# Optimization experiments

Hardware: AMD Instinct MI355X
Metric: run time of the kernel (lower is better)

Reference implementation:

```python
import jax, jax.numpy as jnp
import numpy as np

NUM_SRC1, NUM_DST1 = 2_000_000, 131_072
NUM_SRC2, NUM_DST2 = 131_072, 8_192
E1, E2 = NUM_DST1 * 15, NUM_DST2 * 15
F_IN, F_H = 128, 128


def setup_inputs() -> dict:
    key = jax.random.key(0)
    ks = jax.random.split(key, 10)
    return {
        "x": jax.random.normal(ks[0], (NUM_SRC1, F_IN), dtype=jnp.float32),
        "edge1_src": jax.random.randint(ks[1], (E1,), 0, NUM_SRC1, dtype=jnp.int32),
        "edge1_dst": jax.random.randint(ks[2], (E1,), 0, NUM_DST1, dtype=jnp.int32),
        "edge2_src": jax.random.randint(ks[3], (E2,), 0, NUM_SRC2, dtype=jnp.int32),
        "edge2_dst": jax.random.randint(ks[4], (E2,), 0, NUM_DST2, dtype=jnp.int32),
        "num_dst1": NUM_DST1,
        "num_dst2": NUM_DST2,
        "W_self1": jax.random.normal(ks[5], (F_IN, F_H), dtype=jnp.float32) * 0.05,
        "W_neigh1": jax.random.normal(ks[6], (F_IN, F_H), dtype=jnp.float32) * 0.05,
        "b1": jnp.zeros((F_H,), dtype=jnp.float32),
        "W_self2": jax.random.normal(ks[7], (F_H, F_H), dtype=jnp.float32) * 0.05,
        "W_neigh2": jax.random.normal(ks[8], (F_H, F_H), dtype=jnp.float32) * 0.05,
        "b2": jnp.zeros((F_H,), dtype=jnp.float32),
    }


def _sage_mean(h_src, h_dst, e_src, e_dst, num_dst, W_self, W_neigh, b):
    # mean-aggregate neighbor feats per dst, then linear transforms (DGL SAGEConv, aggr='mean')
    agg = jax.ops.segment_sum(h_src[e_src], e_dst, num_segments=num_dst)  # [num_dst, F]
    deg = jax.ops.segment_sum(jnp.ones((e_dst.shape[0],), h_src.dtype), e_dst,
                              num_segments=num_dst)
    mean = agg / jnp.maximum(deg, 1.0)[:, None]
    return h_dst @ W_self + mean @ W_neigh + b


def reference(x, edge1_src, edge1_dst, edge2_src, edge2_dst, num_dst1, num_dst2,
              W_self1, W_neigh1, b1, W_self2, W_neigh2, b2):
    h_dst = x[:num_dst1]
    h = _sage_mean(x, h_dst, edge1_src, edge1_dst, num_dst1, W_self1, W_neigh1, b1)
    h = jax.nn.relu(h)
    h_dst2 = h[:num_dst2]
    out = _sage_mean(h, h_dst2, edge2_src, edge2_dst, num_dst2, W_self2, W_neigh2, b2)
    return out
```

## Files before the change

### kernel.cpp

```cpp
#include <hip/hip_runtime.h>

static constexpr int FDIM = 128;
static constexpr int ND1  = 131072;
static constexpr int ND2  = 8192;
static constexpr int LDP  = 56;

using bf16x8 = __attribute__((ext_vector_type(8))) short;
using u16x8  = __attribute__((ext_vector_type(8))) unsigned short;
using f32x4  = __attribute__((ext_vector_type(4))) float;

static __device__ __forceinline__ unsigned short f2bf(float f) {
  unsigned u = __float_as_uint(f);
  u = (u + 0x7FFFu + ((u >> 16) & 1u)) >> 16;
  return (unsigned short)u;
}
static __device__ __forceinline__ float bf2f(unsigned short s) {
  return __uint_as_float(((unsigned)s) << 16);
}

__global__ void build_hist(const int* __restrict__ e1d, const int* __restrict__ e2d,
                           int* __restrict__ rs1, int* __restrict__ rs2, int E1, int E2,
                           const float* __restrict__ Ws1, const float* __restrict__ Wn1,
                           unsigned short* __restrict__ Wt1,
                           const float* __restrict__ Ws2, const float* __restrict__ Wn2,
                           unsigned short* __restrict__ Wt2, int nb_hist) {
  if ((int)blockIdx.x >= nb_hist) {
    int t = (blockIdx.x - nb_hist) * 256 + threadIdx.x;
    int which = t >> 15;
    int r = t & 32767;
    int col = r >> 8, k = r & 255;
    const float* Ws = which ? Ws2 : Ws1;
    const float* Wn = which ? Wn2 : Wn1;
    unsigned short* Wt = which ? Wt2 : Wt1;
    float v = (k < 128) ? Ws[k * 128 + col] : Wn[(k - 128) * 128 + col];
    Wt[col * 256 + k] = f2bf(v);
    return;
  }
  const int n1 = E1 >> 2, n2 = E2 >> 2;
  int t = blockIdx.x * 256 + threadIdx.x;
  if (t < n1) {
    int4 d = ((const int4*)e1d)[t];
    atomicAdd(&rs1[d.x], 1); atomicAdd(&rs1[d.y], 1);
    atomicAdd(&rs1[d.z], 1); atomicAdd(&rs1[d.w], 1);
  } else if (t < n1 + n2) {
    int4 d = ((const int4*)e2d)[t - n1];
    atomicAdd(&rs2[d.x], 1); atomicAdd(&rs2[d.y], 1);
    atomicAdd(&rs2[d.z], 1); atomicAdd(&rs2[d.w], 1);
  }
  if (blockIdx.x == 0) {
    int tt = threadIdx.x;
    if (tt < (E1 & 3)) atomicAdd(&rs1[e1d[E1 - 1 - tt]], 1);
    int t2 = tt - 8;
    if (t2 >= 0 && t2 < (E2 & 3)) atomicAdd(&rs2[e2d[E2 - 1 - t2]], 1);
  }
}

__global__ __launch_bounds__(1024) void scan2_kernel(int* __restrict__ c1, int n1,
                                                     int* __restrict__ c2, int n2) {
  int* c = blockIdx.x ? c2 : c1;
  const int n = blockIdx.x ? n2 : n1;
  const int tid = threadIdx.x;
  const int chunk = n >> 10;
  const int base = tid * chunk;
  int s = 0;
  for (int j = 0; j < chunk; j += 4) {
    int4 v = *(const int4*)&c[base + j];
    s += v.x + v.y + v.z + v.w;
  }
  __shared__ int ps[1024];
  ps[tid] = s;
  __syncthreads();
  for (int off = 1; off < 1024; off <<= 1) {
    int v = (tid >= off) ? ps[tid - off] : 0;
    __syncthreads();
    ps[tid] += v;
    __syncthreads();
  }
  int run = (tid == 0) ? 0 : ps[tid - 1];
  for (int j = 0; j < chunk; j += 4) {
    int4 v = *(const int4*)&c[base + j];
    int4 o;
    o.x = run; run += v.x; o.y = run; run += v.y;
    o.z = run; run += v.z; o.w = run; run += v.w;
    *(int4*)&c[base + j] = o;
  }
  if (tid == 1023) c[n] = run;
}

__global__ void fill_all(const int* __restrict__ e1s, const int* __restrict__ e1d,
                         const int* __restrict__ e2s, const int* __restrict__ e2d,
                         const int* __restrict__ rs1, const int* __restrict__ rs2,
                         int* __restrict__ cur1, int* __restrict__ cur2,
                         int* __restrict__ csr1, int* __restrict__ csr2, int E1, int E2) {
  const int n1 = E1 >> 2, n2 = E2 >> 2;
  int t = blockIdx.x * 256 + threadIdx.x;
  if (t < n1) {
    int4 d = ((const int4*)e1d)[t];
    int4 s = ((const int4*)e1s)[t];
    int p;
    p = atomicAdd(&cur1[d.x], 1); csr1[rs1[d.x] + p] = s.x;
    p = atomicAdd(&cur1[d.y], 1); csr1[rs1[d.y] + p] = s.y;
    p = atomicAdd(&cur1[d.z], 1); csr1[rs1[d.z] + p] = s.z;
    p = atomicAdd(&cur1[d.w], 1); csr1[rs1[d.w] + p] = s.w;
  } else if (t < n1 + n2) {
    int4 d = ((const int4*)e2d)[t - n1];
    int4 s = ((const int4*)e2s)[t - n1];
    int p;
    p = atomicAdd(&cur2[d.x], 1); csr2[rs2[d.x] + p] = s.x;
    p = atomicAdd(&cur2[d.y], 1); csr2[rs2[d.y] + p] = s.y;
    p = atomicAdd(&cur2[d.z], 1); csr2[rs2[d.z] + p] = s.z;
    p = atomicAdd(&cur2[d.w], 1); csr2[rs2[d.w] + p] = s.w;
  }
  if (blockIdx.x == 0) {
    int tt = threadIdx.x;
    if (tt < (E1 & 3)) {
      int e = E1 - 1 - tt, d = e1d[e];
      int p = atomicAdd(&cur1[d], 1); csr1[rs1[d] + p] = e1s[e];
    }
    int t2 = tt - 8;
    if (t2 >= 0 && t2 < (E2 & 3)) {
      int e = E2 - 1 - t2, d = e2d[e];
      int p = atomicAdd(&cur2[d], 1); csr2[rs2[d] + p] = e2s[e];
    }
  }
}

__global__ __launch_bounds__(256)
void gather_mean1(const float* __restrict__ src, const int* __restrict__ csr,
                  const int* __restrict__ rs, unsigned short* __restrict__ out, int nrows) {
  const int tid  = threadIdx.x;
  const int lane = tid & 63;
  const int half = lane >> 5;
  const int sub  = lane & 31;
  const int wid  = (int)((blockIdx.x * 256u + tid) >> 6);
  const int row  = wid * 2 + half;
  if (row >= nrows) return;
  const int start = rs[row];
  const int deg   = rs[row + 1] - start;
  float ax = 0.f, ay = 0.f, az = 0.f, aw = 0.f;
  for (int base = 0; base < deg; base += 32) {
    int t = base + sub;
    int idx = csr[start + (t < deg ? t : deg - 1)];
    const int lim = (deg - base) < 32 ? (deg - base) : 32;
    for (int b = 0; b < lim; b += 8) {
      float4 v[8];
      #pragma unroll
      for (int j = 0; j < 8; ++j) {
        int e = __shfl(idx, half * 32 + b + j);
        v[j] = *(const float4*)(src + (size_t)e * FDIM + sub * 4);
      }
      #pragma unroll
      for (int j = 0; j < 8; ++j) {
        float mk = (b + j) < lim ? 1.f : 0.f;
        ax = fmaf(v[j].x, mk, ax); ay = fmaf(v[j].y, mk, ay);
        az = fmaf(v[j].z, mk, az); aw = fmaf(v[j].w, mk, aw);
      }
    }
  }
  const float inv = 1.f / (float)(deg > 1 ? deg : 1);
  ushort4 o;
  o.x = f2bf(ax * inv); o.y = f2bf(ay * inv);
  o.z = f2bf(az * inv); o.w = f2bf(aw * inv);
  *(ushort4*)(out + (size_t)row * FDIM + sub * 4) = o;
}

__global__ __launch_bounds__(256)
void gather_mean2(const unsigned short* __restrict__ src, const int* __restrict__ csr,
                  const int* __restrict__ rs, unsigned short* __restrict__ out, int nrows) {
  const int tid  = threadIdx.x;
  const int lane = tid & 63;
  const int half = lane >> 5;
  const int sub  = lane & 31;
  const int wid  = (int)((blockIdx.x * 256u + tid) >> 6);
  const int row  = wid * 2 + half;
  if (row >= nrows) return;
  const int start = rs[row];
  const int deg   = rs[row + 1] - start;
  float ax = 0.f, ay = 0.f, az = 0.f, aw = 0.f;
  for (int base = 0; base < deg; base += 32) {
    int t = base + sub;
    int idx = csr[start + (t < deg ? t : deg - 1)];
    const int lim = (deg - base) < 32 ? (deg - base) : 32;
    for (int b = 0; b < lim; b += 8) {
      ushort4 v[8];
      #pragma unroll
      for (int j = 0; j < 8; ++j) {
        int e = __shfl(idx, half * 32 + b + j);
        v[j] = *(const ushort4*)(src + (size_t)e * FDIM + sub * 4);
      }
      #pragma unroll
      for (int j = 0; j < 8; ++j) {
        float mk = (b + j) < lim ? 1.f : 0.f;
        ax = fmaf(bf2f(v[j].x), mk, ax); ay = fmaf(bf2f(v[j].y), mk, ay);
        az = fmaf(bf2f(v[j].z), mk, az); aw = fmaf(bf2f(v[j].w), mk, aw);
      }
    }
  }
  const float inv = 1.f / (float)(deg > 1 ? deg : 1);
  ushort4 o;
  o.x = f2bf(ax * inv); o.y = f2bf(ay * inv);
  o.z = f2bf(az * inv); o.w = f2bf(aw * inv);
  *(ushort4*)(out + (size_t)row * FDIM + sub * 4) = o;
}

template<bool RELU, bool AX_BF16, bool OUT_F32>
__global__ __launch_bounds__(256)
void gemm_mfma(const void* __restrict__ Axp,
               const unsigned short* __restrict__ Am,
               const unsigned short* __restrict__ Wt,
               const float* __restrict__ bias,
               void* __restrict__ Outp) {
  __shared__ unsigned short Asb[128 * LDP];
  __shared__ unsigned short Wsb[128 * LDP];
  const int tid  = threadIdx.x;
  const int lane = tid & 63;
  const int w    = tid >> 6;
  const int row0 = blockIdx.x * 128;
  const int p    = lane & 15;
  const int q    = lane >> 4;

  f32x4 acc[2][8];
  #pragma unroll
  for (int m = 0; m < 2; ++m)
    #pragma unroll
    for (int n = 0; n < 8; ++n) acc[m][n] = (f32x4){0.f, 0.f, 0.f, 0.f};

  const int sr = tid >> 1;
  const int sk = (tid & 1) * 16;

  for (int c = 0; c < 8; ++c) {
    const int kc = c * 32;
    const int kl = kc & 127;
    {
      const unsigned short* wsrc = Wt + (size_t)sr * 256 + kc + sk;
      u16x8 a = *(const u16x8*)(wsrc);
      u16x8 b = *(const u16x8*)(wsrc + 8);
      *(u16x8*)&Wsb[sr * LDP + sk]     = a;
      *(u16x8*)&Wsb[sr * LDP + sk + 8] = b;
    }
    if (AX_BF16 || c >= 4) {
      const unsigned short* asrc =
          (c < 4 ? (const unsigned short*)Axp : Am) + (size_t)(row0 + sr) * FDIM + kl + sk;
      u16x8 a = *(const u16x8*)(asrc);
      u16x8 b = *(const u16x8*)(asrc + 8);
      *(u16x8*)&Asb[sr * LDP + sk]     = a;
      *(u16x8*)&Asb[sr * LDP + sk + 8] = b;
    } else {
      const float* asrc = (const float*)Axp + (size_t)(row0 + sr) * FDIM + kl + sk;
      float4 f0 = *(const float4*)(asrc);
      float4 f1 = *(const float4*)(asrc + 4);
      float4 f2 = *(const float4*)(asrc + 8);
      float4 f3 = *(const float4*)(asrc + 12);
      u16x8 a, b;
      a[0] = f2bf(f0.x); a[1] = f2bf(f0.y); a[2] = f2bf(f0.z); a[3] = f2bf(f0.w);
      a[4] = f2bf(f1.x); a[5] = f2bf(f1.y); a[6] = f2bf(f1.z); a[7] = f2bf(f1.w);
      b[0] = f2bf(f2.x); b[1] = f2bf(f2.y); b[2] = f2bf(f2.z); b[3] = f2bf(f2.w);
      b[4] = f2bf(f3.x); b[5] = f2bf(f3.y); b[6] = f2bf(f3.z); b[7] = f2bf(f3.w);
      *(u16x8*)&Asb[sr * LDP + sk]     = a;
      *(u16x8*)&Asb[sr * LDP + sk + 8] = b;
    }
    __syncthreads();
    bf16x8 af[2];
    #pragma unroll
    for (int m = 0; m < 2; ++m)
      af[m] = *(const bf16x8*)&Asb[(w * 32 + m * 16 + p) * LDP + q * 8];
    #pragma unroll
    for (int n = 0; n < 8; ++n) {
      bf16x8 bfr = *(const bf16x8*)&Wsb[(n * 16 + p) * LDP + q * 8];
      acc[0][n] = __builtin_amdgcn_mfma_f32_16x16x32_bf16(af[0], bfr, acc[0][n], 0, 0, 0);
      acc[1][n] = __builtin_amdgcn_mfma_f32_16x16x32_bf16(af[1], bfr, acc[1][n], 0, 0, 0);
    }
    __syncthreads();
  }

  #pragma unroll
  for (int n = 0; n < 8; ++n) {
    const int col = n * 16 + p;
    const float bv = bias[col];
    #pragma unroll
    for (int m = 0; m < 2; ++m) {
      #pragma unroll
      for (int r = 0; r < 4; ++r) {
        float y = acc[m][n][r] + bv;
        if (RELU) y = fmaxf(y, 0.f);
        const size_t grow = (size_t)(row0 + w * 32 + m * 16 + q * 4 + r);
        if (OUT_F32) ((float*)Outp)[grow * FDIM + col] = y;
        else         ((unsigned short*)Outp)[grow * FDIM + col] = f2bf(y);
      }
    }
  }
}

extern "C" void kernel_launch(void* const* d_in, const int* in_sizes, int n_in,
                              void* d_out, int out_size, void* d_ws, size_t ws_size,
                              hipStream_t stream) {
  const float* x   = (const float*)d_in[0];
  const int*   e1s = (const int*)d_in[1];
  const int*   e1d = (const int*)d_in[2];
  const int*   e2s = (const int*)d_in[3];
  const int*   e2d = (const int*)d_in[4];
  const float* Ws1 = (const float*)d_in[7];
  const float* Wn1 = (const float*)d_in[8];
  const float* b1  = (const float*)d_in[9];
  const float* Ws2 = (const float*)d_in[10];
  const float* Wn2 = (const float*)d_in[11];
  const float* b2  = (const float*)d_in[12];
  const int E1 = in_sizes[1];
  const int E2 = in_sizes[3];

  char* pw = (char*)d_ws;
  unsigned short* agg1 = (unsigned short*)pw; pw += (size_t)ND1 * FDIM * 2;
  unsigned short* h    = (unsigned short*)pw; pw += (size_t)ND1 * FDIM * 2;
  unsigned short* agg2 = (unsigned short*)pw; pw += (size_t)ND2 * FDIM * 2;
  unsigned short* Wt1  = (unsigned short*)pw; pw += (size_t)FDIM * 256 * 2;
  unsigned short* Wt2  = (unsigned short*)pw; pw += (size_t)FDIM * 256 * 2;
  int* csr1 = (int*)pw; pw += (size_t)E1 * 4;
  int* csr2 = (int*)pw; pw += (size_t)E2 * 4;
  int* rs1  = (int*)pw; pw += (size_t)(ND1 + 4) * 4;
  int* rs2  = (int*)pw; pw += (size_t)(ND2 + 4) * 4;
  int* cur1 = (int*)pw; pw += (size_t)ND1 * 4;
  int* cur2 = (int*)pw; pw += (size_t)ND2 * 4;
  const size_t ZB = (size_t)(ND1 + 4 + ND2 + 4 + ND1 + ND2) * 4;

  hipMemsetAsync(rs1, 0, ZB, stream);

  const int n4 = (E1 >> 2) + (E2 >> 2);
  const int nb_hist = (n4 + 255) / 256;
  build_hist<<<nb_hist + 256, 256, 0, stream>>>(e1d, e2d, rs1, rs2, E1, E2,
                                                Ws1, Wn1, Wt1, Ws2, Wn2, Wt2, nb_hist);
  scan2_kernel<<<2, 1024, 0, stream>>>(rs1, ND1, rs2, ND2);
  fill_all<<<(n4 + 255) / 256, 256, 0, stream>>>(e1s, e1d, e2s, e2d, rs1, rs2,
                                                 cur1, cur2, csr1, csr2, E1, E2);

  gather_mean1<<<ND1 / 8, 256, 0, stream>>>(x, csr1, rs1, agg1, ND1);
  gemm_mfma<true, false, false><<<ND1 / 128, 256, 0, stream>>>(x, agg1, Wt1, b1, h);

  gather_mean2<<<ND2 / 8, 256, 0, stream>>>(h, csr2, rs2, agg2, ND2);
  gemm_mfma<false, true, true><<<ND2 / 128, 256, 0, stream>>>(h, agg2, Wt2, b2, (float*)d_out);
}
```

Measured before the change: 479.1 us.

## Build CSR in place with shifted offsets; gather one row per wavefront

The histogram now counts into row pointers shifted by four entries. The exclusive scan then leaves start offsets there, and fill_all's atomic increments turn them directly into CSR write positions. This removes the separate cursor arrays, their zeroing, and the per-edge rs reads, and the end-of-scan total write is dropped. The gather kernels change from two rows per wavefront with 16-byte loads to one row per wavefront with 8-byte loads per lane. Loads are predicated, so padded neighbors are no longer fetched. The trade is more wavefronts and smaller per-lane loads.

```diff
diff --git a/kernel.cpp b/kernel.cpp
--- a/kernel.cpp
+++ b/kernel.cpp
@@ -17,6 +17,7 @@
 static __device__ __forceinline__ float bf2f(unsigned short s) {
   return __uint_as_float(((unsigned)s) << 16);
 }
+
 
 __global__ void build_hist(const int* __restrict__ e1d, const int* __restrict__ e2d,
                            int* __restrict__ rs1, int* __restrict__ rs2, int E1, int E2,
@@ -36,28 +37,30 @@
     Wt[col * 256 + k] = f2bf(v);
     return;
   }
+  int* c1 = rs1 + 4;
+  int* c2 = rs2 + 4;
   const int n1 = E1 >> 2, n2 = E2 >> 2;
   int t = blockIdx.x * 256 + threadIdx.x;
   if (t < n1) {
     int4 d = ((const int4*)e1d)[t];
-    atomicAdd(&rs1[d.x], 1); atomicAdd(&rs1[d.y], 1);
-    atomicAdd(&rs1[d.z], 1); atomicAdd(&rs1[d.w], 1);
+    atomicAdd(&c1[d.x], 1); atomicAdd(&c1[d.y], 1);
+    atomicAdd(&c1[d.z], 1); atomicAdd(&c1[d.w], 1);
   } else if (t < n1 + n2) {
     int4 d = ((const int4*)e2d)[t - n1];
-    atomicAdd(&rs2[d.x], 1); atomicAdd(&rs2[d.y], 1);
-    atomicAdd(&rs2[d.z], 1); atomicAdd(&rs2[d.w], 1);
+    atomicAdd(&c2[d.x], 1); atomicAdd(&c2[d.y], 1);
+    atomicAdd(&c2[d.z], 1); atomicAdd(&c2[d.w], 1);
   }
   if (blockIdx.x == 0) {
     int tt = threadIdx.x;
-    if (tt < (E1 & 3)) atomicAdd(&rs1[e1d[E1 - 1 - tt]], 1);
+    if (tt < (E1 & 3)) atomicAdd(&c1[e1d[E1 - 1 - tt]], 1);
     int t2 = tt - 8;
-    if (t2 >= 0 && t2 < (E2 & 3)) atomicAdd(&rs2[e2d[E2 - 1 - t2]], 1);
-  }
-}
-
-__global__ __launch_bounds__(1024) void scan2_kernel(int* __restrict__ c1, int n1,
-                                                     int* __restrict__ c2, int n2) {
-  int* c = blockIdx.x ? c2 : c1;
+    if (t2 >= 0 && t2 < (E2 & 3)) atomicAdd(&c2[e2d[E2 - 1 - t2]], 1);
+  }
+}
+
+__global__ __launch_bounds__(1024) void scan2_kernel(int* __restrict__ rs1, int n1,
+                                                     int* __restrict__ rs2, int n2) {
+  int* c = (blockIdx.x ? rs2 : rs1) + 4;
   const int n = blockIdx.x ? n2 : n1;
   const int tid = threadIdx.x;
   const int chunk = n >> 10;
@@ -84,43 +87,43 @@
     o.z = run; run += v.z; o.w = run; run += v.w;
     *(int4*)&c[base + j] = o;
   }
-  if (tid == 1023) c[n] = run;
 }
 
 __global__ void fill_all(const int* __restrict__ e1s, const int* __restrict__ e1d,
                          const int* __restrict__ e2s, const int* __restrict__ e2d,
-                         const int* __restrict__ rs1, const int* __restrict__ rs2,
-                         int* __restrict__ cur1, int* __restrict__ cur2,
+                         int* __restrict__ rs1, int* __restrict__ rs2,
                          int* __restrict__ csr1, int* __restrict__ csr2, int E1, int E2) {
+  int* c1 = rs1 + 4;
+  int* c2 = rs2 + 4;
   const int n1 = E1 >> 2, n2 = E2 >> 2;
   int t = blockIdx.x * 256 + threadIdx.x;
   if (t < n1) {
     int4 d = ((const int4*)e1d)[t];
     int4 s = ((const int4*)e1s)[t];
     int p;
-    p = atomicAdd(&cur1[d.x], 1); csr1[rs1[d.x] + p] = s.x;
-    p = atomicAdd(&cur1[d.y], 1); csr1[rs1[d.y] + p] = s.y;
-    p = atomicAdd(&cur1[d.z], 1); csr1[rs1[d.z] + p] = s.z;
-    p = atomicAdd(&cur1[d.w], 1); csr1[rs1[d.w] + p] = s.w;
+    p = atomicAdd(&c1[d.x], 1); csr1[p] = s.x;
+    p = atomicAdd(&c1[d.y], 1); csr1[p] = s.y;
+    p = atomicAdd(&c1[d.z], 1); csr1[p] = s.z;
+    p = atomicAdd(&c1[d.w], 1); csr1[p] = s.w;
   } else if (t < n1 + n2) {
     int4 d = ((const int4*)e2d)[t - n1];
     int4 s = ((const int4*)e2s)[t - n1];
     int p;
-    p = atomicAdd(&cur2[d.x], 1); csr2[rs2[d.x] + p] = s.x;
-    p = atomicAdd(&cur2[d.y], 1); csr2[rs2[d.y] + p] = s.y;
-    p = atomicAdd(&cur2[d.z], 1); csr2[rs2[d.z] + p] = s.z;
-    p = atomicAdd(&cur2[d.w], 1); csr2[rs2[d.w] + p] = s.w;
+    p = atomicAdd(&c2[d.x], 1); csr2[p] = s.x;
+    p = atomicAdd(&c2[d.y], 1); csr2[p] = s.y;
+    p = atomicAdd(&c2[d.z], 1); csr2[p] = s.z;
+    p = atomicAdd(&c2[d.w], 1); csr2[p] = s.w;
   }
   if (blockIdx.x == 0) {
     int tt = threadIdx.x;
     if (tt < (E1 & 3)) {
-      int e = E1 - 1 - tt, d = e1d[e];
-      int p = atomicAdd(&cur1[d], 1); csr1[rs1[d] + p] = e1s[e];
+      int e = E1 - 1 - tt;
+      int p = atomicAdd(&c1[e1d[e]], 1); csr1[p] = e1s[e];
     }
     int t2 = tt - 8;
     if (t2 >= 0 && t2 < (E2 & 3)) {
-      int e = E2 - 1 - t2, d = e2d[e];
-      int p = atomicAdd(&cur2[d], 1); csr2[rs2[d] + p] = e2s[e];
+      int e = E2 - 1 - t2;
+      int p = atomicAdd(&c2[e2d[e]], 1); csr2[p] = e2s[e];
     }
   }
 }
@@ -128,79 +131,71 @@
 __global__ __launch_bounds__(256)
 void gather_mean1(const float* __restrict__ src, const int* __restrict__ csr,
                   const int* __restrict__ rs, unsigned short* __restrict__ out, int nrows) {
-  const int tid  = threadIdx.x;
-  const int lane = tid & 63;
-  const int half = lane >> 5;
-  const int sub  = lane & 31;
-  const int wid  = (int)((blockIdx.x * 256u + tid) >> 6);
-  const int row  = wid * 2 + half;
+  const int lane = threadIdx.x & 63;
+  int row = (int)((blockIdx.x * 256u + threadIdx.x) >> 6);
+  row = __builtin_amdgcn_readfirstlane(row);
   if (row >= nrows) return;
-  const int start = rs[row];
-  const int deg   = rs[row + 1] - start;
-  float ax = 0.f, ay = 0.f, az = 0.f, aw = 0.f;
-  for (int base = 0; base < deg; base += 32) {
-    int t = base + sub;
-    int idx = csr[start + (t < deg ? t : deg - 1)];
-    const int lim = (deg - base) < 32 ? (deg - base) : 32;
-    for (int b = 0; b < lim; b += 8) {
-      float4 v[8];
-      #pragma unroll
-      for (int j = 0; j < 8; ++j) {
-        int e = __shfl(idx, half * 32 + b + j);
-        v[j] = *(const float4*)(src + (size_t)e * FDIM + sub * 4);
+  const int start = rs[row + 3];
+  const int deg   = rs[row + 4] - start;
+  float a0 = 0.f, a1 = 0.f;
+  for (int cb = 0; cb < deg; cb += 64) {
+    const int rem0 = deg - cb;
+    const int rem  = rem0 < 64 ? rem0 : 64;
+    int idx = csr[start + cb + (lane < rem ? lane : rem - 1)];
+    for (int base = 0; base < rem; base += 16) {
+      float2 v[16];
+      #pragma unroll
+      for (int j = 0; j < 16; ++j) {
+        if (base + j < rem) {
+          int e = __shfl(idx, base + j);
+          v[j] = *(const float2*)(src + (size_t)e * FDIM + lane * 2);
+        }
       }
       #pragma unroll
-      for (int j = 0; j < 8; ++j) {
-        float mk = (b + j) < lim ? 1.f : 0.f;
-        ax = fmaf(v[j].x, mk, ax); ay = fmaf(v[j].y, mk, ay);
-        az = fmaf(v[j].z, mk, az); aw = fmaf(v[j].w, mk, aw);
-      }
+      for (int j = 0; j < 16; ++j)
+        if (base + j < rem) { a0 += v[j].x; a1 += v[j].y; }
     }
   }
   const float inv = 1.f / (float)(deg > 1 ? deg : 1);
-  ushort4 o;
-  o.x = f2bf(ax * inv); o.y = f2bf(ay * inv);
-  o.z = f2bf(az * inv); o.w = f2bf(aw * inv);
-  *(ushort4*)(out + (size_t)row * FDIM + sub * 4) = o;
+  ushort2 o;
+  o.x = f2bf(a0 * inv);
+  o.y = f2bf(a1 * inv);
+  *(ushort2*)(out + (size_t)row * FDIM + lane * 2) = o;
 }
 
 __global__ __launch_bounds__(256)
 void gather_mean2(const unsigned short* __restrict__ src, const int* __restrict__ csr,
                   const int* __restrict__ rs, unsigned short* __restrict__ out, int nrows) {
-  const int tid  = threadIdx.x;
-  const int lane = tid & 63;
-  const int half = lane >> 5;
-  const int sub  = lane & 31;
-  const int wid  = (int)((blockIdx.x * 256u + tid) >> 6);
-  const int row  = wid * 2 + half;
+  const int lane = threadIdx.x & 63;
+  int row = (int)((blockIdx.x * 256u + threadIdx.x) >> 6);
+  row = __builtin_amdgcn_readfirstlane(row);
   if (row >= nrows) return;
-  const int start = rs[row];
-  const int deg   = rs[row + 1] - start;
-  float ax = 0.f, ay = 0.f, az = 0.f, aw = 0.f;
-  for (int base = 0; base < deg; base += 32) {
-    int t = base + sub;
-    int idx = csr[start + (t < deg ? t : deg - 1)];
-    const int lim = (deg - base) < 32 ? (deg - base) : 32;
-    for (int b = 0; b < lim; b += 8) {
-      ushort4 v[8];
-      #pragma unroll
-      for (int j = 0; j < 8; ++j) {
-        int e = __shfl(idx, half * 32 + b + j);
-        v[j] = *(const ushort4*)(src + (size_t)e * FDIM + sub * 4);
+  const int start = rs[row + 3];
+  const int deg   = rs[row + 4] - start;
+  float a0 = 0.f, a1 = 0.f;
+  for (int cb = 0; cb < deg; cb += 64) {
+    const int rem0 = deg - cb;
+    const int rem  = rem0 < 64 ? rem0 : 64;
+    int idx = csr[start + cb + (lane < rem ? lane : rem - 1)];
+    for (int base = 0; base < rem; base += 16) {
+      ushort2 v[16];
+      #pragma unroll
+      for (int j = 0; j < 16; ++j) {
+        if (base + j < rem) {
+          int e = __shfl(idx, base + j);
+          v[j] = *(const ushort2*)(src + (size_t)e * FDIM + lane * 2);
+        }
       }
       #pragma unroll
-      for (int j = 0; j < 8; ++j) {
-        float mk = (b + j) < lim ? 1.f : 0.f;
-        ax = fmaf(bf2f(v[j].x), mk, ax); ay = fmaf(bf2f(v[j].y), mk, ay);
-        az = fmaf(bf2f(v[j].z), mk, az); aw = fmaf(bf2f(v[j].w), mk, aw);
-      }
+      for (int j = 0; j < 16; ++j)
+        if (base + j < rem) { a0 += bf2f(v[j].x); a1 += bf2f(v[j].y); }
     }
   }
   const float inv = 1.f / (float)(deg > 1 ? deg : 1);
-  ushort4 o;
-  o.x = f2bf(ax * inv); o.y = f2bf(ay * inv);
-  o.z = f2bf(az * inv); o.w = f2bf(aw * inv);
-  *(ushort4*)(out + (size_t)row * FDIM + sub * 4) = o;
+  ushort2 o;
+  o.x = f2bf(a0 * inv);
+  o.y = f2bf(a1 * inv);
+  *(ushort2*)(out + (size_t)row * FDIM + lane * 2) = o;
 }
 
 template<bool RELU, bool AX_BF16, bool OUT_F32>
@@ -316,11 +311,9 @@
   unsigned short* Wt2  = (unsigned short*)pw; pw += (size_t)FDIM * 256 * 2;
   int* csr1 = (int*)pw; pw += (size_t)E1 * 4;
   int* csr2 = (int*)pw; pw += (size_t)E2 * 4;
-  int* rs1  = (int*)pw; pw += (size_t)(ND1 + 4) * 4;
-  int* rs2  = (int*)pw; pw += (size_t)(ND2 + 4) * 4;
-  int* cur1 = (int*)pw; pw += (size_t)ND1 * 4;
-  int* cur2 = (int*)pw; pw += (size_t)ND2 * 4;
-  const size_t ZB = (size_t)(ND1 + 4 + ND2 + 4 + ND1 + ND2) * 4;
+  int* rs1  = (int*)pw; pw += (size_t)(ND1 + 8) * 4;
+  int* rs2  = (int*)pw; pw += (size_t)(ND2 + 8) * 4;
+  const size_t ZB = (size_t)(ND1 + 8 + ND2 + 8) * 4;
 
   hipMemsetAsync(rs1, 0, ZB, stream);
 
@@ -330,11 +323,11 @@
                                                 Ws1, Wn1, Wt1, Ws2, Wn2, Wt2, nb_hist);
   scan2_kernel<<<2, 1024, 0, stream>>>(rs1, ND1, rs2, ND2);
   fill_all<<<(n4 + 255) / 256, 256, 0, stream>>>(e1s, e1d, e2s, e2d, rs1, rs2,
-                                                 cur1, cur2, csr1, csr2, E1, E2);
-
-  gather_mean1<<<ND1 / 8, 256, 0, stream>>>(x, csr1, rs1, agg1, ND1);
+                                                 csr1, csr2, E1, E2);
+
+  gather_mean1<<<ND1 / 4, 256, 0, stream>>>(x, csr1, rs1, agg1, ND1);
   gemm_mfma<true, false, false><<<ND1 / 128, 256, 0, stream>>>(x, agg1, Wt1, b1, h);
 
-  gather_mean2<<<ND2 / 8, 256, 0, stream>>>(h, csr2, rs2, agg2, ND2);
+  gather_mean2<<<ND2 / 4, 256, 0, stream>>>(h, csr2, rs2, agg2, ND2);
   gemm_mfma<false, true, true><<<ND2 / 128, 256, 0, stream>>>(h, agg2, Wt2, b2, (float*)d_out);
 }
```

After: 590.0 us. 1.23x slower.
